# Optimization experiments

Hardware: AMD Instinct MI355X
Metric: run time of the kernel (lower is better)

Reference implementation:

```python
import jax, jax.numpy as jnp
import numpy as np

N, E = 50000, 800000
IN_DIM, HID, OUT_DIM = 128, 64, 64
H1, H2 = 4, 2
LRELU_SLOPE = 0.2
LN_EPS = 1e-5


def _glorot(key, shape):
    fan = shape[0] + shape[-1]
    lim = float(np.sqrt(6.0 / fan))
    return jax.random.uniform(key, shape, jnp.float32, -lim, lim)


def setup_inputs() -> dict:
    key = jax.random.key(0)
    ks = jax.random.split(key, 12)
    x = jax.random.normal(ks[0], (N, IN_DIM), jnp.float32)
    edge_index = jax.random.randint(ks[1], (2, E), 0, N, jnp.int64)
    return {
        "x": x,
        "edge_index": edge_index,
        # layer 1: GATConv(128 -> 64, heads=4, concat=True)
        "W1": _glorot(ks[2], (IN_DIM, H1 * HID)),
        "att_src1": _glorot(ks[3], (H1, HID)),
        "att_dst1": _glorot(ks[4], (H1, HID)),
        "b1": jnp.zeros((H1 * HID,), jnp.float32),
        # LayerNorm(256)
        "ln_w": jnp.ones((H1 * HID,), jnp.float32),
        "ln_b": jnp.zeros((H1 * HID,), jnp.float32),
        # layer 2: GATConv(256 -> 64, heads=2, concat=False)
        "W2": _glorot(ks[5], (H1 * HID, H2 * OUT_DIM)),
        "att_src2": _glorot(ks[6], (H2, OUT_DIM)),
        "att_dst2": _glorot(ks[7], (H2, OUT_DIM)),
        "b2": jnp.zeros((OUT_DIM,), jnp.float32),
    }


def gat_layer(x, src, dst, W, a_src, a_dst, bias, heads, out_ch, concat):
    n = x.shape[0]
    h = (x @ W).reshape(n, heads, out_ch)                 # [N,H,C]
    al_s = jnp.einsum("nhc,hc->nh", h, a_src)             # [N,H]
    al_d = jnp.einsum("nhc,hc->nh", h, a_dst)
    e = jax.nn.leaky_relu(al_s[src] + al_d[dst], LRELU_SLOPE)  # [E,H]
    # segment softmax over incoming edges of each dst node
    m = jax.ops.segment_max(e, dst, num_segments=n)
    e = jnp.exp(e - m[dst])
    denom = jax.ops.segment_sum(e, dst, num_segments=n)
    alpha = e / denom[dst]                                # [E,H]
    msg = h[src] * alpha[:, :, None]                      # [E,H,C]
    out = jax.ops.segment_sum(msg, dst, num_segments=n)   # [N,H,C]
    out = out.reshape(n, heads * out_ch) if concat else out.mean(axis=1)
    return out + bias


def layer_norm(x, w, b):
    mu = x.mean(axis=-1, keepdims=True)
    var = ((x - mu) ** 2).mean(axis=-1, keepdims=True)
    return (x - mu) * jax.lax.rsqrt(var + LN_EPS) * w + b


def reference(x, edge_index, W1, att_src1, att_dst1, b1, ln_w, ln_b,
              W2, att_src2, att_dst2, b2):
    # PyG GATConv adds self-loops by default
    loops = jnp.arange(N, dtype=edge_index.dtype)
    src = jnp.concatenate([edge_index[0], loops])
    dst = jnp.concatenate([edge_index[1], loops])
    h = gat_layer(x, src, dst, W1, att_src1, att_dst1, b1, H1, HID, True)
    h = layer_norm(h, ln_w, ln_b)
    h = jax.nn.elu(h)
    # dropout is identity in eval mode
    h = gat_layer(h, src, dst, W2, att_src2, att_dst2, b2, H2, OUT_DIM, False)
    return h
```

## Files before the change

kernel.cpp:

```cpp
#include <hip/hip_runtime.h>
#include <hip/hip_bf16.h>
#include <math.h>

#define IN_DIM  128
#define HID     64
#define H1      4
#define H2      2
#define OUT_DIM 64
#define D1      256
#define D2      128
#define LRELU   0.2f
#define LN_EPS  1e-5f

using short8 = __attribute__((ext_vector_type(8))) short;
using f32x4  = __attribute__((ext_vector_type(4))) float;

static __device__ __forceinline__ unsigned short f2bf_bits(float f)
{
    __hip_bfloat16 b = __float2bfloat16(f);
    return *reinterpret_cast<unsigned short*>(&b);
}
static __device__ __forceinline__ float2 unpack_bf2(unsigned int p)
{
    float2 r;
    r.x = __uint_as_float(p << 16);
    r.y = __uint_as_float(p & 0xffff0000u);
    return r;
}
static __device__ __forceinline__ unsigned int pack_bf2(float x, float y)
{
    return (unsigned int)f2bf_bits(x) | ((unsigned int)f2bf_bits(y) << 16);
}

template<int H>
static __device__ __forceinline__ float edge_w(
    const float* __restrict__ al_s, int src, float ad, int h)
{
    float v = al_s[(size_t)src * H + h] + ad;
    v = v > 0.f ? v : LRELU * v;
    return __expf(v);
}

static __device__ __forceinline__ int detect_i64(const int* __restrict__ ei)
{
    int any_odd_nonzero = 0;
    #pragma unroll
    for (int k = 1; k < 16; k += 2) any_odd_nonzero |= (ei[k] != 0);
    return any_odd_nonzero ? 0 : 1;
}

__global__ __launch_bounds__(256) void conv_hist_kernel(
    const float* __restrict__ W1, const float* __restrict__ W2,
    unsigned short* __restrict__ Wp1, unsigned short* __restrict__ Wp2,
    const int* __restrict__ ei, int E, int* __restrict__ deg)
{
    const int bid = blockIdx.x;
    if (bid < 256) {
        int tid = bid * 256 + threadIdx.x;
        if (tid < 32768) {
            int j = tid & 7, l = (tid >> 3) & 63, rest = tid >> 9;
            int s = rest & 15, t = rest >> 4;
            int k = t * 32 + (l >> 4) * 8 + j, col = s * 16 + (l & 15);
            Wp1[tid] = f2bf_bits(W1[k * D1 + col]);
        } else {
            int id = tid - 32768;
            int j = id & 7, l = (id >> 3) & 63, rest = id >> 9;
            int s = rest & 7, t = rest >> 3;
            int k = t * 32 + (l >> 4) * 8 + j, col = s * 16 + (l & 15);
            Wp2[id] = f2bf_bits(W2[k * D2 + col]);
        }
    } else {
        const int i64f = detect_i64(ei);
        int e = (bid - 256) * 256 + threadIdx.x;
        if (e >= E) return;
        int dst = i64f ? ei[2 * ((size_t)E + e)] : ei[E + e];
        atomicAdd(&deg[dst], 1);
    }
}

__global__ __launch_bounds__(256) void scan_partial(
    const int* __restrict__ deg, int N, int* __restrict__ bsum)
{
    __shared__ int s[256];
    int i = blockIdx.x * 256 + threadIdx.x;
    s[threadIdx.x] = (i < N) ? deg[i] : 0;
    __syncthreads();
    for (int st = 128; st > 0; st >>= 1) {
        if (threadIdx.x < st) s[threadIdx.x] += s[threadIdx.x + st];
        __syncthreads();
    }
    if (threadIdx.x == 0) bsum[blockIdx.x] = s[0];
}

__global__ __launch_bounds__(256) void scan_final(
    const int* __restrict__ deg, const int* __restrict__ bsum, int B, int N, int E,
    int* __restrict__ rowptr, int* __restrict__ cursor)
{
    __shared__ int sb[256];
    __shared__ int s[256];
    sb[threadIdx.x] = (threadIdx.x < B) ? bsum[threadIdx.x] : 0;
    __syncthreads();
    for (int st = 1; st < 256; st <<= 1) {
        int t = (threadIdx.x >= st) ? sb[threadIdx.x - st] : 0;
        __syncthreads();
        sb[threadIdx.x] += t;
        __syncthreads();
    }
    const int blockOff = (blockIdx.x == 0) ? 0 : sb[blockIdx.x - 1];

    int i = blockIdx.x * 256 + threadIdx.x;
    int v = (i < N) ? deg[i] : 0;
    s[threadIdx.x] = v;
    __syncthreads();
    for (int st = 1; st < 256; st <<= 1) {
        int t = (threadIdx.x >= st) ? s[threadIdx.x - st] : 0;
        __syncthreads();
        s[threadIdx.x] += t;
        __syncthreads();
    }
    int excl = s[threadIdx.x] - v + blockOff;
    if (i < N) { rowptr[i] = excl; cursor[i] = excl; }
    if (blockIdx.x == 0 && threadIdx.x == 0) rowptr[N] = E;
}

__global__ __launch_bounds__(256) void fill_kernel(
    const int* __restrict__ ei, int E,
    int* __restrict__ cursor, int* __restrict__ csr_src)
{
    const int i64f = detect_i64(ei);
    int e = blockIdx.x * 256 + threadIdx.x;
    if (e >= E) return;
    int src, dst;
    if (i64f) { src = ei[2 * (size_t)e]; dst = ei[2 * ((size_t)E + e)]; }
    else      { src = ei[e];             dst = ei[E + e]; }
    int pos = atomicAdd(&cursor[dst], 1);
    csr_src[pos] = src;
}

__global__ __launch_bounds__(256) void gemm1_mfma(
    const float* __restrict__ x, const unsigned short* __restrict__ Wp,
    const float* __restrict__ att_s, const float* __restrict__ att_d,
    unsigned short* __restrict__ h1b,
    float* __restrict__ al_s, float* __restrict__ al_d, int N)
{
    __shared__ __align__(16) unsigned short As[16 * 136];
    const int tid = threadIdx.x;
    const int n0 = blockIdx.x * 16;
    const int l = tid & 63, w = tid >> 6;

    #pragma unroll
    for (int it = 0; it < 2; ++it) {
        int ch = tid + it * 256;
        int r = ch >> 5, c4 = (ch & 31) * 4;
        int row = n0 + r;
        float4 v = (row < N) ? ((const float4*)x)[(size_t)row * 32 + (c4 >> 2)]
                             : make_float4(0.f, 0.f, 0.f, 0.f);
        ushort4 pk = make_ushort4(f2bf_bits(v.x), f2bf_bits(v.y),
                                  f2bf_bits(v.z), f2bf_bits(v.w));
        *(ushort4*)&As[r * 136 + c4] = pk;
    }

    short8 bfr[4][4];
    #pragma unroll
    for (int t = 0; t < 4; ++t)
        #pragma unroll
        for (int p = 0; p < 4; ++p)
            bfr[t][p] = ((const short8*)Wp)[(t * 16 + (w * 4 + p)) * 64 + l];

    __syncthreads();

    f32x4 acc[4] = {{0.f,0.f,0.f,0.f},{0.f,0.f,0.f,0.f},
                    {0.f,0.f,0.f,0.f},{0.f,0.f,0.f,0.f}};
    #pragma unroll
    for (int t = 0; t < 4; ++t) {
        short8 a = *(const short8*)&As[(l & 15) * 136 + t * 32 + (l >> 4) * 8];
        #pragma unroll
        for (int p = 0; p < 4; ++p)
            acc[p] = __builtin_amdgcn_mfma_f32_16x16x32_bf16(a, bfr[t][p], acc[p], 0, 0, 0);
    }

    const int colbase = w * 64 + (l & 15);
    const int rowbase = n0 + (l >> 4) * 4;
    #pragma unroll
    for (int p = 0; p < 4; ++p) {
        int col = colbase + p * 16;
        #pragma unroll
        for (int r = 0; r < 4; ++r) {
            int row = rowbase + r;
            if (row < N) h1b[(size_t)row * D1 + col] = f2bf_bits(acc[p][r]);
        }
    }

    float as_p[4], ad_p[4];
    #pragma unroll
    for (int p = 0; p < 4; ++p) {
        as_p[p] = att_s[colbase + p * 16];
        ad_p[p] = att_d[colbase + p * 16];
    }
    #pragma unroll
    for (int r = 0; r < 4; ++r) {
        float ps = acc[0][r] * as_p[0] + acc[1][r] * as_p[1]
                 + acc[2][r] * as_p[2] + acc[3][r] * as_p[3];
        float pd = acc[0][r] * ad_p[0] + acc[1][r] * ad_p[1]
                 + acc[2][r] * ad_p[2] + acc[3][r] * ad_p[3];
        #pragma unroll
        for (int off = 8; off > 0; off >>= 1) {
            ps += __shfl_down(ps, off);
            pd += __shfl_down(pd, off);
        }
        int row = rowbase + r;
        if ((l & 15) == 0 && row < N) {
            al_s[(size_t)row * H1 + w] = ps;
            al_d[(size_t)row * H1 + w] = pd;
        }
    }
}

__global__ __launch_bounds__(256) void gemm2_mfma(
    const unsigned short* __restrict__ hmidb, const unsigned short* __restrict__ Wp,
    const float* __restrict__ att_s, const float* __restrict__ att_d,
    unsigned short* __restrict__ h2b,
    float* __restrict__ al_s, float* __restrict__ al_d, int N)
{
    __shared__ __align__(16) unsigned short As[16 * 264];
    __shared__ float psL[4][16], pdL[4][16];
    const int tid = threadIdx.x;
    const int n0 = blockIdx.x * 16;
    const int l = tid & 63, w = tid >> 6;

    const short8 zero8 = {0,0,0,0,0,0,0,0};
    #pragma unroll
    for (int it = 0; it < 2; ++it) {
        int ch = tid + it * 256;
        int r = ch >> 5, c8 = (ch & 31) * 8;
        int row = n0 + r;
        short8 v = (row < N) ? ((const short8*)hmidb)[(size_t)row * 32 + (ch & 31)] : zero8;
        *(short8*)&As[r * 264 + c8] = v;
    }

    short8 bfr[8][2];
    #pragma unroll
    for (int t = 0; t < 8; ++t)
        #pragma unroll
        for (int q = 0; q < 2; ++q)
            bfr[t][q] = ((const short8*)Wp)[(t * 8 + (w * 2 + q)) * 64 + l];

    __syncthreads();

    f32x4 acc[2] = {{0.f,0.f,0.f,0.f},{0.f,0.f,0.f,0.f}};
    #pragma unroll
    for (int t = 0; t < 8; ++t) {
        short8 a = *(const short8*)&As[(l & 15) * 264 + t * 32 + (l >> 4) * 8];
        #pragma unroll
        for (int q = 0; q < 2; ++q)
            acc[q] = __builtin_amdgcn_mfma_f32_16x16x32_bf16(a, bfr[t][q], acc[q], 0, 0, 0);
    }

    const int colbase = w * 32 + (l & 15);
    const int rowbase = n0 + (l >> 4) * 4;
    #pragma unroll
    for (int q = 0; q < 2; ++q) {
        int col = colbase + q * 16;
        #pragma unroll
        for (int r = 0; r < 4; ++r) {
            int row = rowbase + r;
            if (row < N) h2b[(size_t)row * D2 + col] = f2bf_bits(acc[q][r]);
        }
    }

    float as_q[2], ad_q[2];
    #pragma unroll
    for (int q = 0; q < 2; ++q) {
        as_q[q] = att_s[colbase + q * 16];
        ad_q[q] = att_d[colbase + q * 16];
    }
    #pragma unroll
    for (int r = 0; r < 4; ++r) {
        float ps = acc[0][r] * as_q[0] + acc[1][r] * as_q[1];
        float pd = acc[0][r] * ad_q[0] + acc[1][r] * ad_q[1];
        #pragma unroll
        for (int off = 8; off > 0; off >>= 1) {
            ps += __shfl_down(ps, off);
            pd += __shfl_down(pd, off);
        }
        if ((l & 15) == 0) {
            psL[w][(l >> 4) * 4 + r] = ps;
            pdL[w][(l >> 4) * 4 + r] = pd;
        }
    }
    __syncthreads();
    if (tid < 32) {
        int rl = tid & 15, hh = tid >> 4;
        int row = n0 + rl;
        if (row < N) {
            al_s[(size_t)row * H2 + hh] = psL[2*hh][rl] + psL[2*hh+1][rl];
            al_d[(size_t)row * H2 + hh] = pdL[2*hh][rl] + pdL[2*hh+1][rl];
        }
    }
}

__global__ __launch_bounds__(64) void agg1_kernel(
    const int* __restrict__ rowptr, const int* __restrict__ csr_src,
    const uint2* __restrict__ h1p,
    const float* __restrict__ al_s, const float* __restrict__ al_d,
    const float* __restrict__ b1,
    const float* __restrict__ ln_w, const float* __restrict__ ln_b,
    uint2* __restrict__ hmidp, int N)
{
    const int n = blockIdx.x;
    const int t = threadIdx.x;
    const int h = t >> 4;
    const float ad = al_d[(size_t)n * H1 + h];

    float a0[4] = {0.f,0.f,0.f,0.f}, a1[4] = {0.f,0.f,0.f,0.f};
    float a2[4] = {0.f,0.f,0.f,0.f}, a3[4] = {0.f,0.f,0.f,0.f};
    float dn0, dn1 = 0.f, dn2 = 0.f, dn3 = 0.f;

    {
        float w = edge_w<H1>(al_s, n, ad, h);
        uint2 p = h1p[(size_t)n * 64 + t];
        float2 va = unpack_bf2(p.x), vb = unpack_bf2(p.y);
        a0[0] = w * va.x; a0[1] = w * va.y; a0[2] = w * vb.x; a0[3] = w * vb.y;
        dn0 = w;
    }

    const int beg = rowptr[n], end = rowptr[n + 1];
    int i = beg;

#define LOADE1(k) int s##k = csr_src[i + k]; \
                  uint2 p##k = h1p[(size_t)s##k * 64 + t]; \
                  float w##k = edge_w<H1>(al_s, s##k, ad, h);
#define ACC1(A, D, k) { float2 va = unpack_bf2(p##k.x), vb = unpack_bf2(p##k.y); \
                        A[0] += w##k * va.x; A[1] += w##k * va.y; \
                        A[2] += w##k * vb.x; A[3] += w##k * vb.y; D += w##k; }

    for (; i + 8 <= end; i += 8) {
        LOADE1(0) LOADE1(1) LOADE1(2) LOADE1(3)
        LOADE1(4) LOADE1(5) LOADE1(6) LOADE1(7)
        ACC1(a0, dn0, 0) ACC1(a1, dn1, 1) ACC1(a2, dn2, 2) ACC1(a3, dn3, 3)
        ACC1(a0, dn0, 4) ACC1(a1, dn1, 5) ACC1(a2, dn2, 6) ACC1(a3, dn3, 7)
    }
    for (; i + 4 <= end; i += 4) {
        LOADE1(0) LOADE1(1) LOADE1(2) LOADE1(3)
        ACC1(a0, dn0, 0) ACC1(a1, dn1, 1) ACC1(a2, dn2, 2) ACC1(a3, dn3, 3)
    }
    for (; i < end; ++i) {
        LOADE1(0) ACC1(a0, dn0, 0)
    }
#undef LOADE1
#undef ACC1

    const float inv = 1.f / ((dn0 + dn1) + (dn2 + dn3));
    float4 bb = ((const float4*)b1)[t];
    float v[4];
    v[0] = ((a0[0]+a1[0]) + (a2[0]+a3[0])) * inv + bb.x;
    v[1] = ((a0[1]+a1[1]) + (a2[1]+a3[1])) * inv + bb.y;
    v[2] = ((a0[2]+a1[2]) + (a2[2]+a3[2])) * inv + bb.z;
    v[3] = ((a0[3]+a1[3]) + (a2[3]+a3[3])) * inv + bb.w;

    float s  = (v[0]+v[1]) + (v[2]+v[3]);
    float s2 = (v[0]*v[0]+v[1]*v[1]) + (v[2]*v[2]+v[3]*v[3]);
    #pragma unroll
    for (int off = 32; off > 0; off >>= 1) {
        s  += __shfl_down(s,  off);
        s2 += __shfl_down(s2, off);
    }
    const float mu   = __shfl(s,  0) * (1.f / 256.f);
    const float ex2  = __shfl(s2, 0) * (1.f / 256.f);
    const float rstd = rsqrtf(ex2 - mu * mu + LN_EPS);
    float4 lw = ((const float4*)ln_w)[t];
    float4 lb = ((const float4*)ln_b)[t];
    float y0 = (v[0] - mu) * rstd * lw.x + lb.x;
    float y1 = (v[1] - mu) * rstd * lw.y + lb.y;
    float y2 = (v[2] - mu) * rstd * lw.z + lb.z;
    float y3 = (v[3] - mu) * rstd * lw.w + lb.w;
    y0 = y0 > 0.f ? y0 : (__expf(y0) - 1.f);
    y1 = y1 > 0.f ? y1 : (__expf(y1) - 1.f);
    y2 = y2 > 0.f ? y2 : (__expf(y2) - 1.f);
    y3 = y3 > 0.f ? y3 : (__expf(y3) - 1.f);
    uint2 outp;
    outp.x = pack_bf2(y0, y1);
    outp.y = pack_bf2(y2, y3);
    hmidp[(size_t)n * 64 + t] = outp;
}

__global__ __launch_bounds__(64) void agg2_kernel(
    const int* __restrict__ rowptr, const int* __restrict__ csr_src,
    const unsigned int* __restrict__ h2p,
    const float* __restrict__ al_s, const float* __restrict__ al_d,
    const float* __restrict__ b2,
    float* __restrict__ out, int N)
{
    const int n = blockIdx.x;
    const int t = threadIdx.x;
    const int h = t >> 5;
    const float ad = al_d[(size_t)n * H2 + h];

    float ax0, ay0, dn0;
    float ax1 = 0.f, ay1 = 0.f, dn1 = 0.f;
    float ax2 = 0.f, ay2 = 0.f, dn2 = 0.f;
    float ax3 = 0.f, ay3 = 0.f, dn3 = 0.f;
    {
        float w = edge_w<H2>(al_s, n, ad, h);
        float2 hv = unpack_bf2(h2p[(size_t)n * 64 + t]);
        ax0 = w * hv.x; ay0 = w * hv.y; dn0 = w;
    }

    const int beg = rowptr[n], end = rowptr[n + 1];
    int i = beg;

#define LOADE2(k) int s##k = csr_src[i + k]; \
                  unsigned int p##k = h2p[(size_t)s##k * 64 + t]; \
                  float w##k = edge_w<H2>(al_s, s##k, ad, h);
#define ACC2(AX, AY, D, k) { float2 vv = unpack_bf2(p##k); \
                             AX += w##k * vv.x; AY += w##k * vv.y; D += w##k; }

    for (; i + 8 <= end; i += 8) {
        LOADE2(0) LOADE2(1) LOADE2(2) LOADE2(3)
        LOADE2(4) LOADE2(5) LOADE2(6) LOADE2(7)
        ACC2(ax0, ay0, dn0, 0) ACC2(ax1, ay1, dn1, 1)
        ACC2(ax2, ay2, dn2, 2) ACC2(ax3, ay3, dn3, 3)
        ACC2(ax0, ay0, dn0, 4) ACC2(ax1, ay1, dn1, 5)
        ACC2(ax2, ay2, dn2, 6) ACC2(ax3, ay3, dn3, 7)
    }
    for (; i + 4 <= end; i += 4) {
        LOADE2(0) LOADE2(1) LOADE2(2) LOADE2(3)
        ACC2(ax0, ay0, dn0, 0) ACC2(ax1, ay1, dn1, 1)
        ACC2(ax2, ay2, dn2, 2) ACC2(ax3, ay3, dn3, 3)
    }
    for (; i < end; ++i) {
        LOADE2(0) ACC2(ax0, ay0, dn0, 0)
    }
#undef LOADE2
#undef ACC2

    const float inv = 1.f / ((dn0 + dn1) + (dn2 + dn3));
    const float vx = ((ax0 + ax1) + (ax2 + ax3)) * inv;
    const float vy = ((ay0 + ay1) + (ay2 + ay3)) * inv;

    __shared__ float sv[128];
    sv[2 * t]     = vx;
    sv[2 * t + 1] = vy;
    __syncthreads();
    out[(size_t)n * OUT_DIM + t] = 0.5f * (sv[t] + sv[64 + t]) + b2[t];
}

extern "C" void kernel_launch(void* const* d_in, const int* in_sizes, int n_in,
                              void* d_out, int out_size, void* d_ws, size_t ws_size,
                              hipStream_t stream)
{
    const float* x   = (const float*)d_in[0];
    const int*   ei  = (const int*)d_in[1];
    const float* W1  = (const float*)d_in[2];
    const float* as1 = (const float*)d_in[3];
    const float* ad1 = (const float*)d_in[4];
    const float* b1  = (const float*)d_in[5];
    const float* lnw = (const float*)d_in[6];
    const float* lnb = (const float*)d_in[7];
    const float* W2  = (const float*)d_in[8];
    const float* as2 = (const float*)d_in[9];
    const float* ad2 = (const float*)d_in[10];
    const float* b2  = (const float*)d_in[11];

    const int N = in_sizes[0] / IN_DIM;
    const int E = in_sizes[1] / 2;

    char* ws = (char*)d_ws;
    const size_t szH1b = (size_t)N * D1 * sizeof(unsigned short);
    unsigned short* h1b   = (unsigned short*)(ws);
    unsigned short* hmidb = (unsigned short*)(ws + szH1b);
    unsigned short* Wp1   = (unsigned short*)(ws + 2 * szH1b);
    unsigned short* Wp2   = Wp1 + 32768;
    float* al_s1 = (float*)(Wp2 + 32768);
    float* al_d1 = al_s1 + (size_t)N * H1;
    float* al_s2 = al_d1 + (size_t)N * H1;
    float* al_d2 = al_s2 + (size_t)N * H2;
    int* deg     = (int*)(al_d2 + (size_t)N * H2);
    int* rowptr  = deg + (N + 1);
    int* cursor  = rowptr + (N + 1);
    int* csr_src = cursor + (N + 1);
    int* bsum    = csr_src + E;
    unsigned short* h2b = h1b;

    hipMemsetAsync(deg, 0, (size_t)(N + 1) * sizeof(int), stream);

    const int edgeBlocks = (E + 255) / 256;
    const int scanBlocks = (N + 255) / 256;
    const int tileBlocks = (N + 15) / 16;

    conv_hist_kernel<<<256 + edgeBlocks, 256, 0, stream>>>(W1, W2, Wp1, Wp2, ei, E, deg);
    scan_partial<<<scanBlocks, 256, 0, stream>>>(deg, N, bsum);
    scan_final<<<scanBlocks, 256, 0, stream>>>(deg, bsum, scanBlocks, N, E, rowptr, cursor);
    fill_kernel<<<edgeBlocks, 256, 0, stream>>>(ei, E, cursor, csr_src);

    gemm1_mfma<<<tileBlocks, 256, 0, stream>>>(x, Wp1, as1, ad1, h1b, al_s1, al_d1, N);
    agg1_kernel<<<N, 64, 0, stream>>>(rowptr, csr_src, (const uint2*)h1b,
                                      al_s1, al_d1, b1, lnw, lnb,
                                      (uint2*)hmidb, N);
    gemm2_mfma<<<tileBlocks, 256, 0, stream>>>(hmidb, Wp2, as2, ad2, h2b, al_s2, al_d2, N);
    agg2_kernel<<<N, 64, 0, stream>>>(rowptr, csr_src, (const unsigned int*)h2b,
                                      al_s2, al_d2, b2, (float*)d_out, N);
}
```

Measured before the change: 314.0 us.

## Fuse degree scan with gemm1 and pack four nodes per aggregation block

Merges the partial degree scan and the first GEMM into one launch, with the scan blocks reusing the GEMM shared buffer. This removes a kernel launch and lets the GEMM run alongside the scan. The aggregation kernels now process four destination nodes per 256-thread block, one wavefront each, instead of one 64-thread block per node, which is meant to cut block scheduling overhead. The 8-wide unrolled edge loops are dropped, and agg2's head average uses a wave shuffle instead of shared memory and a barrier, which may reduce memory-level parallelism on high-degree nodes.

```diff
diff --git a/kernel.cpp b/kernel.cpp
--- a/kernel.cpp
+++ b/kernel.cpp
@@ -78,18 +78,98 @@
     }
 }
 
-__global__ __launch_bounds__(256) void scan_partial(
-    const int* __restrict__ deg, int N, int* __restrict__ bsum)
-{
-    __shared__ int s[256];
-    int i = blockIdx.x * 256 + threadIdx.x;
-    s[threadIdx.x] = (i < N) ? deg[i] : 0;
+__global__ __launch_bounds__(256) void scan_gemm1_kernel(
+    const int* __restrict__ deg, int N, int* __restrict__ bsum, int scanB,
+    const float* __restrict__ x, const unsigned short* __restrict__ Wp,
+    const float* __restrict__ att_s, const float* __restrict__ att_d,
+    unsigned short* __restrict__ h1b,
+    float* __restrict__ al_s, float* __restrict__ al_d)
+{
+    __shared__ __align__(16) unsigned short As[16 * 136];
+    const int tid = threadIdx.x;
+
+    if ((int)blockIdx.x < scanB) {
+        int* s = (int*)As;
+        int i = blockIdx.x * 256 + tid;
+        s[tid] = (i < N) ? deg[i] : 0;
+        __syncthreads();
+        for (int st = 128; st > 0; st >>= 1) {
+            if (tid < st) s[tid] += s[tid + st];
+            __syncthreads();
+        }
+        if (tid == 0) bsum[blockIdx.x] = s[0];
+        return;
+    }
+
+    const int n0 = ((int)blockIdx.x - scanB) * 16;
+    const int l = tid & 63, w = tid >> 6;
+
+    #pragma unroll
+    for (int it = 0; it < 2; ++it) {
+        int ch = tid + it * 256;
+        int r = ch >> 5, c4 = (ch & 31) * 4;
+        int row = n0 + r;
+        float4 v = (row < N) ? ((const float4*)x)[(size_t)row * 32 + (c4 >> 2)]
+                             : make_float4(0.f, 0.f, 0.f, 0.f);
+        ushort4 pk = make_ushort4(f2bf_bits(v.x), f2bf_bits(v.y),
+                                  f2bf_bits(v.z), f2bf_bits(v.w));
+        *(ushort4*)&As[r * 136 + c4] = pk;
+    }
+
+    short8 bfr[4][4];
+    #pragma unroll
+    for (int t = 0; t < 4; ++t)
+        #pragma unroll
+        for (int p = 0; p < 4; ++p)
+            bfr[t][p] = ((const short8*)Wp)[(t * 16 + (w * 4 + p)) * 64 + l];
+
     __syncthreads();
-    for (int st = 128; st > 0; st >>= 1) {
-        if (threadIdx.x < st) s[threadIdx.x] += s[threadIdx.x + st];
-        __syncthreads();
-    }
-    if (threadIdx.x == 0) bsum[blockIdx.x] = s[0];
+
+    f32x4 acc[4] = {{0.f,0.f,0.f,0.f},{0.f,0.f,0.f,0.f},
+                    {0.f,0.f,0.f,0.f},{0.f,0.f,0.f,0.f}};
+    #pragma unroll
+    for (int t = 0; t < 4; ++t) {
+        short8 a = *(const short8*)&As[(l & 15) * 136 + t * 32 + (l >> 4) * 8];
+        #pragma unroll
+        for (int p = 0; p < 4; ++p)
+            acc[p] = __builtin_amdgcn_mfma_f32_16x16x32_bf16(a, bfr[t][p], acc[p], 0, 0, 0);
+    }
+
+    const int colbase = w * 64 + (l & 15);
+    const int rowbase = n0 + (l >> 4) * 4;
+    #pragma unroll
+    for (int p = 0; p < 4; ++p) {
+        int col = colbase + p * 16;
+        #pragma unroll
+        for (int r = 0; r < 4; ++r) {
+            int row = rowbase + r;
+            if (row < N) h1b[(size_t)row * D1 + col] = f2bf_bits(acc[p][r]);
+        }
+    }
+
+    float as_p[4], ad_p[4];
+    #pragma unroll
+    for (int p = 0; p < 4; ++p) {
+        as_p[p] = att_s[colbase + p * 16];
+        ad_p[p] = att_d[colbase + p * 16];
+    }
+    #pragma unroll
+    for (int r = 0; r < 4; ++r) {
+        float ps = acc[0][r] * as_p[0] + acc[1][r] * as_p[1]
+                 + acc[2][r] * as_p[2] + acc[3][r] * as_p[3];
+        float pd = acc[0][r] * ad_p[0] + acc[1][r] * ad_p[1]
+                 + acc[2][r] * ad_p[2] + acc[3][r] * ad_p[3];
+        #pragma unroll
+        for (int off = 8; off > 0; off >>= 1) {
+            ps += __shfl_down(ps, off);
+            pd += __shfl_down(pd, off);
+        }
+        int row = rowbase + r;
+        if ((l & 15) == 0 && row < N) {
+            al_s[(size_t)row * H1 + w] = ps;
+            al_d[(size_t)row * H1 + w] = pd;
+        }
+    }
 }
 
 __global__ __launch_bounds__(256) void scan_final(
@@ -137,85 +217,6 @@
     csr_src[pos] = src;
 }
 
-__global__ __launch_bounds__(256) void gemm1_mfma(
-    const float* __restrict__ x, const unsigned short* __restrict__ Wp,
-    const float* __restrict__ att_s, const float* __restrict__ att_d,
-    unsigned short* __restrict__ h1b,
-    float* __restrict__ al_s, float* __restrict__ al_d, int N)
-{
-    __shared__ __align__(16) unsigned short As[16 * 136];
-    const int tid = threadIdx.x;
-    const int n0 = blockIdx.x * 16;
-    const int l = tid & 63, w = tid >> 6;
-
-    #pragma unroll
-    for (int it = 0; it < 2; ++it) {
-        int ch = tid + it * 256;
-        int r = ch >> 5, c4 = (ch & 31) * 4;
-        int row = n0 + r;
-        float4 v = (row < N) ? ((const float4*)x)[(size_t)row * 32 + (c4 >> 2)]
-                             : make_float4(0.f, 0.f, 0.f, 0.f);
-        ushort4 pk = make_ushort4(f2bf_bits(v.x), f2bf_bits(v.y),
-                                  f2bf_bits(v.z), f2bf_bits(v.w));
-        *(ushort4*)&As[r * 136 + c4] = pk;
-    }
-
-    short8 bfr[4][4];
-    #pragma unroll
-    for (int t = 0; t < 4; ++t)
-        #pragma unroll
-        for (int p = 0; p < 4; ++p)
-            bfr[t][p] = ((const short8*)Wp)[(t * 16 + (w * 4 + p)) * 64 + l];
-
-    __syncthreads();
-
-    f32x4 acc[4] = {{0.f,0.f,0.f,0.f},{0.f,0.f,0.f,0.f},
-                    {0.f,0.f,0.f,0.f},{0.f,0.f,0.f,0.f}};
-    #pragma unroll
-    for (int t = 0; t < 4; ++t) {
-        short8 a = *(const short8*)&As[(l & 15) * 136 + t * 32 + (l >> 4) * 8];
-        #pragma unroll
-        for (int p = 0; p < 4; ++p)
-            acc[p] = __builtin_amdgcn_mfma_f32_16x16x32_bf16(a, bfr[t][p], acc[p], 0, 0, 0);
-    }
-
-    const int colbase = w * 64 + (l & 15);
-    const int rowbase = n0 + (l >> 4) * 4;
-    #pragma unroll
-    for (int p = 0; p < 4; ++p) {
-        int col = colbase + p * 16;
-        #pragma unroll
-        for (int r = 0; r < 4; ++r) {
-            int row = rowbase + r;
-            if (row < N) h1b[(size_t)row * D1 + col] = f2bf_bits(acc[p][r]);
-        }
-    }
-
-    float as_p[4], ad_p[4];
-    #pragma unroll
-    for (int p = 0; p < 4; ++p) {
-        as_p[p] = att_s[colbase + p * 16];
-        ad_p[p] = att_d[colbase + p * 16];
-    }
-    #pragma unroll
-    for (int r = 0; r < 4; ++r) {
-        float ps = acc[0][r] * as_p[0] + acc[1][r] * as_p[1]
-                 + acc[2][r] * as_p[2] + acc[3][r] * as_p[3];
-        float pd = acc[0][r] * ad_p[0] + acc[1][r] * ad_p[1]
-                 + acc[2][r] * ad_p[2] + acc[3][r] * ad_p[3];
-        #pragma unroll
-        for (int off = 8; off > 0; off >>= 1) {
-            ps += __shfl_down(ps, off);
-            pd += __shfl_down(pd, off);
-        }
-        int row = rowbase + r;
-        if ((l & 15) == 0 && row < N) {
-            al_s[(size_t)row * H1 + w] = ps;
-            al_d[(size_t)row * H1 + w] = pd;
-        }
-    }
-}
-
 __global__ __launch_bounds__(256) void gemm2_mfma(
     const unsigned short* __restrict__ hmidb, const unsigned short* __restrict__ Wp,
     const float* __restrict__ att_s, const float* __restrict__ att_d,
@@ -299,7 +300,7 @@
     }
 }
 
-__global__ __launch_bounds__(64) void agg1_kernel(
+__global__ __launch_bounds__(256) void agg1_kernel(
     const int* __restrict__ rowptr, const int* __restrict__ csr_src,
     const uint2* __restrict__ h1p,
     const float* __restrict__ al_s, const float* __restrict__ al_d,
@@ -307,9 +308,10 @@
     const float* __restrict__ ln_w, const float* __restrict__ ln_b,
     uint2* __restrict__ hmidp, int N)
 {
-    const int n = blockIdx.x;
-    const int t = threadIdx.x;
-    const int h = t >> 4;
+    const int n = blockIdx.x * 4 + (threadIdx.x >> 6);
+    if (n >= N) return;
+    const int l = threadIdx.x & 63;
+    const int h = l >> 4;
     const float ad = al_d[(size_t)n * H1 + h];
 
     float a0[4] = {0.f,0.f,0.f,0.f}, a1[4] = {0.f,0.f,0.f,0.f};
@@ -318,7 +320,7 @@
 
     {
         float w = edge_w<H1>(al_s, n, ad, h);
-        uint2 p = h1p[(size_t)n * 64 + t];
+        uint2 p = h1p[(size_t)n * 64 + l];
         float2 va = unpack_bf2(p.x), vb = unpack_bf2(p.y);
         a0[0] = w * va.x; a0[1] = w * va.y; a0[2] = w * vb.x; a0[3] = w * vb.y;
         dn0 = w;
@@ -328,18 +330,12 @@
     int i = beg;
 
 #define LOADE1(k) int s##k = csr_src[i + k]; \
-                  uint2 p##k = h1p[(size_t)s##k * 64 + t]; \
+                  uint2 p##k = h1p[(size_t)s##k * 64 + l]; \
                   float w##k = edge_w<H1>(al_s, s##k, ad, h);
 #define ACC1(A, D, k) { float2 va = unpack_bf2(p##k.x), vb = unpack_bf2(p##k.y); \
                         A[0] += w##k * va.x; A[1] += w##k * va.y; \
                         A[2] += w##k * vb.x; A[3] += w##k * vb.y; D += w##k; }
 
-    for (; i + 8 <= end; i += 8) {
-        LOADE1(0) LOADE1(1) LOADE1(2) LOADE1(3)
-        LOADE1(4) LOADE1(5) LOADE1(6) LOADE1(7)
-        ACC1(a0, dn0, 0) ACC1(a1, dn1, 1) ACC1(a2, dn2, 2) ACC1(a3, dn3, 3)
-        ACC1(a0, dn0, 4) ACC1(a1, dn1, 5) ACC1(a2, dn2, 6) ACC1(a3, dn3, 7)
-    }
     for (; i + 4 <= end; i += 4) {
         LOADE1(0) LOADE1(1) LOADE1(2) LOADE1(3)
         ACC1(a0, dn0, 0) ACC1(a1, dn1, 1) ACC1(a2, dn2, 2) ACC1(a3, dn3, 3)
@@ -351,7 +347,7 @@
 #undef ACC1
 
     const float inv = 1.f / ((dn0 + dn1) + (dn2 + dn3));
-    float4 bb = ((const float4*)b1)[t];
+    float4 bb = ((const float4*)b1)[l];
     float v[4];
     v[0] = ((a0[0]+a1[0]) + (a2[0]+a3[0])) * inv + bb.x;
     v[1] = ((a0[1]+a1[1]) + (a2[1]+a3[1])) * inv + bb.y;
@@ -368,8 +364,8 @@
     const float mu   = __shfl(s,  0) * (1.f / 256.f);
     const float ex2  = __shfl(s2, 0) * (1.f / 256.f);
     const float rstd = rsqrtf(ex2 - mu * mu + LN_EPS);
-    float4 lw = ((const float4*)ln_w)[t];
-    float4 lb = ((const float4*)ln_b)[t];
+    float4 lw = ((const float4*)ln_w)[l];
+    float4 lb = ((const float4*)ln_b)[l];
     float y0 = (v[0] - mu) * rstd * lw.x + lb.x;
     float y1 = (v[1] - mu) * rstd * lw.y + lb.y;
     float y2 = (v[2] - mu) * rstd * lw.z + lb.z;
@@ -381,19 +377,20 @@
     uint2 outp;
     outp.x = pack_bf2(y0, y1);
     outp.y = pack_bf2(y2, y3);
-    hmidp[(size_t)n * 64 + t] = outp;
-}
-
-__global__ __launch_bounds__(64) void agg2_kernel(
+    hmidp[(size_t)n * 64 + l] = outp;
+}
+
+__global__ __launch_bounds__(256) void agg2_kernel(
     const int* __restrict__ rowptr, const int* __restrict__ csr_src,
     const unsigned int* __restrict__ h2p,
     const float* __restrict__ al_s, const float* __restrict__ al_d,
     const float* __restrict__ b2,
     float* __restrict__ out, int N)
 {
-    const int n = blockIdx.x;
-    const int t = threadIdx.x;
-    const int h = t >> 5;
+    const int n = blockIdx.x * 4 + (threadIdx.x >> 6);
+    if (n >= N) return;
+    const int l = threadIdx.x & 63;
+    const int h = l >> 5;
     const float ad = al_d[(size_t)n * H2 + h];
 
     float ax0, ay0, dn0;
@@ -402,7 +399,7 @@
     float ax3 = 0.f, ay3 = 0.f, dn3 = 0.f;
     {
         float w = edge_w<H2>(al_s, n, ad, h);
-        float2 hv = unpack_bf2(h2p[(size_t)n * 64 + t]);
+        float2 hv = unpack_bf2(h2p[(size_t)n * 64 + l]);
         ax0 = w * hv.x; ay0 = w * hv.y; dn0 = w;
     }
 
@@ -410,19 +407,11 @@
     int i = beg;
 
 #define LOADE2(k) int s##k = csr_src[i + k]; \
-                  unsigned int p##k = h2p[(size_t)s##k * 64 + t]; \
+                  unsigned int p##k = h2p[(size_t)s##k * 64 + l]; \
                   float w##k = edge_w<H2>(al_s, s##k, ad, h);
 #define ACC2(AX, AY, D, k) { float2 vv = unpack_bf2(p##k); \
                              AX += w##k * vv.x; AY += w##k * vv.y; D += w##k; }
 
-    for (; i + 8 <= end; i += 8) {
-        LOADE2(0) LOADE2(1) LOADE2(2) LOADE2(3)
-        LOADE2(4) LOADE2(5) LOADE2(6) LOADE2(7)
-        ACC2(ax0, ay0, dn0, 0) ACC2(ax1, ay1, dn1, 1)
-        ACC2(ax2, ay2, dn2, 2) ACC2(ax3, ay3, dn3, 3)
-        ACC2(ax0, ay0, dn0, 4) ACC2(ax1, ay1, dn1, 5)
-        ACC2(ax2, ay2, dn2, 6) ACC2(ax3, ay3, dn3, 7)
-    }
     for (; i + 4 <= end; i += 4) {
         LOADE2(0) LOADE2(1) LOADE2(2) LOADE2(3)
         ACC2(ax0, ay0, dn0, 0) ACC2(ax1, ay1, dn1, 1)
@@ -438,11 +427,15 @@
     const float vx = ((ax0 + ax1) + (ax2 + ax3)) * inv;
     const float vy = ((ay0 + ay1) + (ay2 + ay3)) * inv;
 
-    __shared__ float sv[128];
-    sv[2 * t]     = vx;
-    sv[2 * t + 1] = vy;
-    __syncthreads();
-    out[(size_t)n * OUT_DIM + t] = 0.5f * (sv[t] + sv[64 + t]) + b2[t];
+    const float vx1 = __shfl(vx, l + 32);
+    const float vy1 = __shfl(vy, l + 32);
+    if (l < 32) {
+        float2 bb = ((const float2*)b2)[l];
+        float2 o;
+        o.x = 0.5f * (vx + vx1) + bb.x;
+        o.y = 0.5f * (vy + vy1) + bb.y;
+        ((float2*)out)[(size_t)n * 32 + l] = o;
+    }
 }
 
 extern "C" void kernel_launch(void* const* d_in, const int* in_sizes, int n_in,
@@ -487,17 +480,18 @@
     const int edgeBlocks = (E + 255) / 256;
     const int scanBlocks = (N + 255) / 256;
     const int tileBlocks = (N + 15) / 16;
+    const int aggBlocks  = (N + 3) / 4;
 
     conv_hist_kernel<<<256 + edgeBlocks, 256, 0, stream>>>(W1, W2, Wp1, Wp2, ei, E, deg);
-    scan_partial<<<scanBlocks, 256, 0, stream>>>(deg, N, bsum);
+    scan_gemm1_kernel<<<scanBlocks + tileBlocks, 256, 0, stream>>>(
+        deg, N, bsum, scanBlocks, x, Wp1, as1, ad1, h1b, al_s1, al_d1);
     scan_final<<<scanBlocks, 256, 0, stream>>>(deg, bsum, scanBlocks, N, E, rowptr, cursor);
     fill_kernel<<<edgeBlocks, 256, 0, stream>>>(ei, E, cursor, csr_src);
 
-    gemm1_mfma<<<tileBlocks, 256, 0, stream>>>(x, Wp1, as1, ad1, h1b, al_s1, al_d1, N);
-    agg1_kernel<<<N, 64, 0, stream>>>(rowptr, csr_src, (const uint2*)h1b,
-                                      al_s1, al_d1, b1, lnw, lnb,
-                                      (uint2*)hmidb, N);
+    agg1_kernel<<<aggBlocks, 256, 0, stream>>>(rowptr, csr_src, (const uint2*)h1b,
+                                               al_s1, al_d1, b1, lnw, lnb,
+                                               (uint2*)hmidb, N);
     gemm2_mfma<<<tileBlocks, 256, 0, stream>>>(hmidb, Wp2, as2, ad2, h2b, al_s2, al_d2, N);
-    agg2_kernel<<<N, 64, 0, stream>>>(rowptr, csr_src, (const unsigned int*)h2b,
-                                      al_s2, al_d2, b2, (float*)d_out, N);
-}
+    agg2_kernel<<<aggBlocks, 256, 0, stream>>>(rowptr, csr_src, (const unsigned int*)h2b,
+                                               al_s2, al_d2, b2, (float*)d_out, N);
+}
```

Result: slower. 323.7 us (+3.1%).
